# Kernel optimization log

Hardware: AMD Instinct MI355X
Metric: run time of the kernel (lower is better)

## Reference

```python
import jax, jax.numpy as jnp
import numpy as np

NUM_HEADS = 16
HIDDEN = 1024
ATTN_DIM = 64            # per-head q/k dim
HEAD_OUT = 64            # per-head v dim
OUT_DIM = 1024
BATCH, SEQ = 2, 2048


def setup_inputs() -> dict:
    key = jax.random.key(0)
    ks = jax.random.split(key, 9)
    s_in = 1.0 / np.sqrt(HIDDEN)
    s_o = 1.0 / np.sqrt(NUM_HEADS * HEAD_OUT)
    return {
        "x": jax.random.normal(ks[0], (BATCH, SEQ, HIDDEN), dtype=jnp.float32),
        # Linear weights stored [in, out] so y = x @ W + b
        "Wq": jax.random.uniform(ks[1], (HIDDEN, NUM_HEADS * ATTN_DIM), jnp.float32, -s_in, s_in),
        "bq": jax.random.uniform(ks[2], (NUM_HEADS * ATTN_DIM,), jnp.float32, -s_in, s_in),
        "Wk": jax.random.uniform(ks[3], (HIDDEN, NUM_HEADS * ATTN_DIM), jnp.float32, -s_in, s_in),
        "bk": jax.random.uniform(ks[4], (NUM_HEADS * ATTN_DIM,), jnp.float32, -s_in, s_in),
        "Wv": jax.random.uniform(ks[5], (HIDDEN, NUM_HEADS * HEAD_OUT), jnp.float32, -s_in, s_in),
        "bv": jax.random.uniform(ks[6], (HIDDEN, NUM_HEADS * HEAD_OUT)[1:], jnp.float32, -s_in, s_in),
        "Wo": jax.random.uniform(ks[7], (NUM_HEADS * HEAD_OUT, OUT_DIM), jnp.float32, -s_o, s_o),
        "bo": jax.random.uniform(ks[8], (OUT_DIM,), jnp.float32, -s_o, s_o),
    }


def _split_heads(y, h):
    b, s, _ = y.shape
    return y.reshape(b, s, h, -1).transpose(0, 2, 1, 3)  # [b, h, s, d]


def reference(x, Wq, bq, Wk, bk, Wv, bv, Wo, bo):
    h = NUM_HEADS
    q = _split_heads(x @ Wq + bq, h)                    # [b,h,s,dq]
    k = _split_heads(x @ Wk + bk, h)                    # [b,h,s,dq]
    v = _split_heads(x @ Wv + bv, h)                    # [b,h,s,dv]
    scale = 1.0 / jnp.sqrt(jnp.float32(ATTN_DIM))
    # pattern[b,h,i,j] = key_i . query_j  (i=key index, j=query index)
    pattern = jnp.einsum('bhid,bhjd->bhij', k, q) * scale
    # softmax over key axis (dim=-2), matching t.softmax(..., dim=-2)
    prob = jax.nn.softmax(pattern, axis=-2)             # [b,h,key,query]
    # out[b,h,s,d] = sum_i prob[b,h,i,s] * v[b,h,i,d]
    out = jnp.einsum('bhis,bhid->bhsd', prob, v)        # [b,h,s,dv]
    b, _, s, dv = out.shape
    concat = out.transpose(0, 2, 1, 3).reshape(b, s, h * dv)
    return concat @ Wo + bo
```

## Files before the change

### kernel.cpp

```cpp
#include <hip/hip_runtime.h>
#include <cstdint>
#include <cstddef>

using f16   = _Float16;
using f16x4 = __attribute__((ext_vector_type(4))) _Float16;
using f16x8 = __attribute__((ext_vector_type(8))) _Float16;
using f32x4 = __attribute__((ext_vector_type(4))) float;

__device__ __forceinline__ f32x4 mfma16(f16x8 a, f16x8 b, f32x4 c) {
  return __builtin_amdgcn_mfma_f32_16x16x32_f16(a, b, c, 0, 0, 0);
}

__device__ __forceinline__ void gld16(const f16* g, f16* l) {
  __builtin_amdgcn_global_load_lds(
      (__attribute__((address_space(1))) void*)g,
      (__attribute__((address_space(3))) void*)l, 16, 0, 0);
}

constexpr int BATCH = 2, SEQL = 2048, HID = 1024, NH = 16, DH = 64;
constexpr int TOK = BATCH * SEQL;
constexpr int NQKV = 3 * HID;

__global__ __launch_bounds__(256) void k_convert_x(const float* __restrict__ x,
                                                   f16* __restrict__ xh) {
  int i = (blockIdx.x * 256 + threadIdx.x) * 4;
  float4 v = *(const float4*)(x + i);
  f16x4 o = { (f16)v.x, (f16)v.y, (f16)v.z, (f16)v.w };
  *(f16x4*)(xh + i) = o;
}

__global__ __launch_bounds__(256) void k_transpose(const float* __restrict__ Wq,
                                                   const float* __restrict__ Wk,
                                                   const float* __restrict__ Wv,
                                                   const float* __restrict__ Wo,
                                                   f16* __restrict__ WT,
                                                   f16* __restrict__ WoT) {
  __shared__ float tile[32][33];
  int mat = blockIdx.z;
  const float* W = (mat == 0) ? Wq : (mat == 1) ? Wk : (mat == 2) ? Wv : Wo;
  int in0 = blockIdx.x * 32, out0 = blockIdx.y * 32;
  int c = threadIdx.x & 31, r8 = threadIdx.x >> 5;
#pragma unroll
  for (int i = 0; i < 4; i++) {
    int r = r8 + i * 8;
    tile[r][c] = W[(size_t)(in0 + r) * HID + out0 + c];
  }
  __syncthreads();
#pragma unroll
  for (int i = 0; i < 4; i++) {
    int r = r8 + i * 8;
    f16 v = (f16)tile[c][r];
    if (mat == 3) WoT[(size_t)(out0 + r) * HID + in0 + c] = v;
    else          WT[(size_t)(mat * HID + out0 + r) * HID + in0 + c] = v;
  }
}

__global__ __launch_bounds__(256, 2) void k_gemm_qkv(
    const f16* __restrict__ xh, const f16* __restrict__ WT,
    const float* __restrict__ bq, const float* __restrict__ bk,
    const float* __restrict__ bv,
    f16* __restrict__ Qh, f16* __restrict__ Kh, f16* __restrict__ Vth) {
  constexpr int K = HID;
  int m0 = blockIdx.x * 128, n0 = blockIdx.y * 128;
  int tid = threadIdx.x;
  int w = tid >> 6, lane = tid & 63, lr = lane & 15, lq = lane >> 4;
  int wm = w >> 1, wn = w & 1;
  __shared__ f16 Ash[128 * 32];
  __shared__ f16 Bsh[128 * 32];
  f32x4 acc[4][4];
#pragma unroll
  for (int i = 0; i < 4; i++)
#pragma unroll
    for (int j = 0; j < 4; j++) acc[i][j] = (f32x4){0.f, 0.f, 0.f, 0.f};

  int row0 = tid >> 2, seg0 = tid & 3;
  int row1 = (256 + tid) >> 2;
  const f16* Ag0 = xh + (size_t)(m0 + row0) * K + seg0 * 8;
  const f16* Ag1 = xh + (size_t)(m0 + row1) * K + seg0 * 8;
  const f16* Bg0 = WT + (size_t)(n0 + row0) * K + seg0 * 8;
  const f16* Bg1 = WT + (size_t)(n0 + row1) * K + seg0 * 8;

  for (int k0 = 0; k0 < K; k0 += 32) {
    __syncthreads();
    gld16(Ag0 + k0, Ash + tid * 8);
    gld16(Ag1 + k0, Ash + (256 + tid) * 8);
    gld16(Bg0 + k0, Bsh + tid * 8);
    gld16(Bg1 + k0, Bsh + (256 + tid) * 8);
    __syncthreads();
    f16x8 af[4], bfr[4];
#pragma unroll
    for (int mt = 0; mt < 4; mt++)
      af[mt] = *(const f16x8*)(Ash + (wm * 64 + mt * 16 + lr) * 32 + lq * 8);
#pragma unroll
    for (int nt = 0; nt < 4; nt++)
      bfr[nt] = *(const f16x8*)(Bsh + (wn * 64 + nt * 16 + lr) * 32 + lq * 8);
#pragma unroll
    for (int mt = 0; mt < 4; mt++)
#pragma unroll
      for (int nt = 0; nt < 4; nt++)
        acc[mt][nt] = mfma16(af[mt], bfr[nt], acc[mt][nt]);
  }

#pragma unroll
  for (int nt = 0; nt < 4; nt++) {
    int o = n0 + wn * 64 + nt * 16 + lr;
    int sec = o >> 10, o1 = o & 1023, hh = o1 >> 6, dd = o1 & 63;
    float bias = (sec == 0) ? bq[o1] : (sec == 1) ? bk[o1] : bv[o1];
#pragma unroll
    for (int mt = 0; mt < 4; mt++) {
      int t0 = m0 + wm * 64 + mt * 16 + lq * 4;
      int b = t0 >> 11, s0 = t0 & (SEQL - 1);
      size_t bh = (size_t)(b * NH + hh);
      if (sec == 2) {
        f16x4 pv = { (f16)(acc[mt][nt][0] + bias), (f16)(acc[mt][nt][1] + bias),
                     (f16)(acc[mt][nt][2] + bias), (f16)(acc[mt][nt][3] + bias) };
        *(f16x4*)(Vth + (bh * DH + dd) * SEQL + s0) = pv;
      } else {
        f16* dst = (sec == 0) ? Qh : Kh;
#pragma unroll
        for (int r = 0; r < 4; r++)
          dst[(bh * SEQL + s0 + r) * DH + dd] = (f16)(acc[mt][nt][r] + bias);
      }
    }
  }
}

__global__ __launch_bounds__(256, 4) void k_attn(const f16* __restrict__ Qh,
                                                 const f16* __restrict__ Kh,
                                                 const f16* __restrict__ Vth,
                                                 f16* __restrict__ Ao) {
  int qblk = blockIdx.x;
  int bh = blockIdx.y;
  int b = bh >> 4, h = bh & 15;
  int tid = threadIdx.x, w = tid >> 6, lane = tid & 63, lr = lane & 15, lq = lane >> 4;

  __shared__ f16 Ksh[64 * 72];
  __shared__ f16 Vsh[64 * 72];

  int q = qblk * 64 + w * 16 + lr;
  const f16* Qbase = Qh + ((size_t)bh * SEQL + q) * DH;
  f16x8 qf[2];
#pragma unroll
  for (int ks = 0; ks < 2; ks++) {
    qf[ks] = *(const f16x8*)(Qbase + ks * 32 + lq * 8);
    qf[ks] = qf[ks] * (f16)0.125f;
  }

  f32x4 O[4];
#pragma unroll
  for (int dt = 0; dt < 4; dt++) O[dt] = (f32x4){0.f, 0.f, 0.f, 0.f};
  float lsum = 0.f;

  int srow = tid >> 3, sseg = tid & 7;
  int srow1 = (256 + tid) >> 3;
  const f16* Kg0 = Kh + ((size_t)bh * SEQL + srow) * DH + sseg * 8;
  const f16* Kg1 = Kh + ((size_t)bh * SEQL + srow1) * DH + sseg * 8;
  const f16* Vg0 = Vth + ((size_t)bh * DH + srow) * SEQL + sseg * 8;
  const f16* Vg1 = Vth + ((size_t)bh * DH + srow1) * SEQL + sseg * 8;

  for (int kb = 0; kb < SEQL / 64; kb++) {
    __syncthreads();
    *(uint4*)(Ksh + srow * 72 + sseg * 8)  = *(const uint4*)(Kg0 + (size_t)kb * 64 * DH);
    *(uint4*)(Ksh + srow1 * 72 + sseg * 8) = *(const uint4*)(Kg1 + (size_t)kb * 64 * DH);
    *(uint4*)(Vsh + srow * 72 + sseg * 8)  = *(const uint4*)(Vg0 + kb * 64);
    *(uint4*)(Vsh + srow1 * 72 + sseg * 8) = *(const uint4*)(Vg1 + kb * 64);
    __syncthreads();

    f32x4 sacc[4];
#pragma unroll
    for (int kt = 0; kt < 4; kt++) sacc[kt] = (f32x4){0.f, 0.f, 0.f, 0.f};
#pragma unroll
    for (int ks = 0; ks < 2; ks++) {
#pragma unroll
      for (int kt = 0; kt < 4; kt++) {
        f16x8 kf = *(const f16x8*)(Ksh + (kt * 16 + lr) * 72 + ks * 32 + lq * 8);
        sacc[kt] = mfma16(kf, qf[ks], sacc[kt]);
      }
    }

    f16x8 pf[2];
    float part = 0.f;
#pragma unroll
    for (int kt = 0; kt < 4; kt++) {
      float p0 = __expf(sacc[kt][0]);
      float p1 = __expf(sacc[kt][1]);
      float p2 = __expf(sacc[kt][2]);
      float p3 = __expf(sacc[kt][3]);
      part += (p0 + p1) + (p2 + p3);
      int s = kt >> 1, off = (kt & 1) * 4;
      pf[s][off + 0] = (f16)p0; pf[s][off + 1] = (f16)p1;
      pf[s][off + 2] = (f16)p2; pf[s][off + 3] = (f16)p3;
    }
    lsum += part;

#pragma unroll
    for (int s = 0; s < 2; s++) {
#pragma unroll
      for (int dt = 0; dt < 4; dt++) {
        const f16* vb = Vsh + (dt * 16 + lr) * 72 + s * 32 + lq * 4;
        f16x4 v0 = *(const f16x4*)(vb);
        f16x4 v1 = *(const f16x4*)(vb + 16);
        f16x8 vf = { v0[0], v0[1], v0[2], v0[3], v1[0], v1[1], v1[2], v1[3] };
        O[dt] = mfma16(vf, pf[s], O[dt]);
      }
    }
  }

  float l1 = lsum + __shfl_xor(lsum, 16);
  float ltot = l1 + __shfl_xor(l1, 32);
  float inv = 1.0f / ltot;
  f16* dst = Ao + ((size_t)b * SEQL + q) * HID + h * DH;
#pragma unroll
  for (int dt = 0; dt < 4; dt++) {
    f16x4 o = { (f16)(O[dt][0] * inv), (f16)(O[dt][1] * inv),
                (f16)(O[dt][2] * inv), (f16)(O[dt][3] * inv) };
    *(f16x4*)(dst + dt * 16 + lq * 4) = o;
  }
}

__global__ __launch_bounds__(256, 2) void k_gemm_out(const f16* __restrict__ Ah,
                                                     const f16* __restrict__ WoT,
                                                     const float* __restrict__ bo,
                                                     float* __restrict__ out) {
  constexpr int K = HID;
  int m0 = blockIdx.x * 128, n0 = blockIdx.y * 64;
  int tid = threadIdx.x;
  int w = tid >> 6, lane = tid & 63, lr = lane & 15, lq = lane >> 4;
  int wm = w >> 1, wn = w & 1;
  __shared__ f16 Ash[128 * 32];
  __shared__ f16 Bsh[64 * 32];
  f32x4 acc[4][2];
#pragma unroll
  for (int i = 0; i < 4; i++)
#pragma unroll
    for (int j = 0; j < 2; j++) acc[i][j] = (f32x4){0.f, 0.f, 0.f, 0.f};

  int row0 = tid >> 2, seg0 = tid & 3;
  int row1 = (256 + tid) >> 2;
  const f16* Ag0 = Ah + (size_t)(m0 + row0) * K + seg0 * 8;
  const f16* Ag1 = Ah + (size_t)(m0 + row1) * K + seg0 * 8;
  const f16* Bg0 = WoT + (size_t)(n0 + row0) * K + seg0 * 8;

  for (int k0 = 0; k0 < K; k0 += 32) {
    __syncthreads();
    gld16(Ag0 + k0, Ash + tid * 8);
    gld16(Ag1 + k0, Ash + (256 + tid) * 8);
    gld16(Bg0 + k0, Bsh + tid * 8);
    __syncthreads();
    f16x8 af[4], bfr[2];
#pragma unroll
    for (int mt = 0; mt < 4; mt++)
      af[mt] = *(const f16x8*)(Ash + (wm * 64 + mt * 16 + lr) * 32 + lq * 8);
#pragma unroll
    for (int nt = 0; nt < 2; nt++)
      bfr[nt] = *(const f16x8*)(Bsh + (wn * 32 + nt * 16 + lr) * 32 + lq * 8);
#pragma unroll
    for (int mt = 0; mt < 4; mt++)
#pragma unroll
      for (int nt = 0; nt < 2; nt++)
        acc[mt][nt] = mfma16(af[mt], bfr[nt], acc[mt][nt]);
  }

#pragma unroll
  for (int nt = 0; nt < 2; nt++) {
    int o = n0 + wn * 32 + nt * 16 + lr;
    float bias = bo[o];
#pragma unroll
    for (int mt = 0; mt < 4; mt++) {
      int t0 = m0 + wm * 64 + mt * 16 + lq * 4;
#pragma unroll
      for (int r = 0; r < 4; r++)
        out[(size_t)(t0 + r) * HID + o] = acc[mt][nt][r] + bias;
    }
  }
}

extern "C" void kernel_launch(void* const* d_in, const int* in_sizes, int n_in,
                              void* d_out, int out_size, void* d_ws, size_t ws_size,
                              hipStream_t stream) {
  const float* x  = (const float*)d_in[0];
  const float* Wq = (const float*)d_in[1];
  const float* bq = (const float*)d_in[2];
  const float* Wk = (const float*)d_in[3];
  const float* bk = (const float*)d_in[4];
  const float* Wv = (const float*)d_in[5];
  const float* bv = (const float*)d_in[6];
  const float* Wo = (const float*)d_in[7];
  const float* bo = (const float*)d_in[8];

  char* ws = (char*)d_ws;
  f16* xh  = (f16*)(ws + 0);
  f16* WT  = (f16*)(ws + 8388608);
  f16* WoT = (f16*)(ws + 14680064);
  f16* Qh  = (f16*)(ws + 16777216);
  f16* Kh  = (f16*)(ws + 25165824);
  f16* Vth = (f16*)(ws + 33554432);
  f16* Ao  = (f16*)(ws + 41943040);

  k_convert_x<<<TOK * HID / 1024, 256, 0, stream>>>(x, xh);
  k_transpose<<<dim3(32, 32, 4), 256, 0, stream>>>(Wq, Wk, Wv, Wo, WT, WoT);
  k_gemm_qkv<<<dim3(TOK / 128, NQKV / 128), 256, 0, stream>>>(xh, WT, bq, bk, bv,
                                                              Qh, Kh, Vth);
  k_attn<<<dim3(SEQL / 64, BATCH * NH), 256, 0, stream>>>(Qh, Kh, Vth, Ao);
  k_gemm_out<<<dim3(TOK / 128, HID / 64), 256, 0, stream>>>(Ao, WoT, bo,
                                                            (float*)d_out);
}
```

Measured before the change: 207.5 us.

## Double-buffer attention K/V tiles, process two query tiles per wave, permute V layout

The attention kernel now handles 128 queries per block, with each wave computing two 16-query tiles that share the same K and V fragments loaded from LDS. K/V loads are register-prefetched into a double-buffered LDS tile, which removes one barrier per iteration. The V layout written by the QKV GEMM is permuted so the PV operand becomes one contiguous 8-element LDS load instead of two 4-element loads. exp is replaced with exp2 by folding log2(e) into the Q scale. The cost is more registers and lower occupancy, with launch bounds reduced to 2 blocks per SM, and the grid is reordered so that blockIdx.x indexes the head.

```diff
diff --git a/kernel.cpp b/kernel.cpp
--- a/kernel.cpp
+++ b/kernel.cpp
@@ -59,7 +59,7 @@
     const f16* __restrict__ xh, const f16* __restrict__ WT,
     const float* __restrict__ bq, const float* __restrict__ bk,
     const float* __restrict__ bv,
-    f16* __restrict__ Qh, f16* __restrict__ Kh, f16* __restrict__ Vth) {
+    f16* __restrict__ Qh, f16* __restrict__ Kh, f16* __restrict__ Vp) {
   constexpr int K = HID;
   int m0 = blockIdx.x * 128, n0 = blockIdx.y * 128;
   int tid = threadIdx.x;
@@ -114,7 +114,8 @@
       if (sec == 2) {
         f16x4 pv = { (f16)(acc[mt][nt][0] + bias), (f16)(acc[mt][nt][1] + bias),
                      (f16)(acc[mt][nt][2] + bias), (f16)(acc[mt][nt][3] + bias) };
-        *(f16x4*)(Vth + (bh * DH + dd) * SEQL + s0) = pv;
+        int pb = (s0 & ~31) | ((s0 & 12) << 1) | ((s0 >> 2) & 4);
+        *(f16x4*)(Vp + (bh * DH + dd) * SEQL + pb) = pv;
       } else {
         f16* dst = (sec == 0) ? Qh : Kh;
 #pragma unroll
@@ -125,96 +126,120 @@
   }
 }
 
-__global__ __launch_bounds__(256, 4) void k_attn(const f16* __restrict__ Qh,
+__global__ __launch_bounds__(256, 2) void k_attn(const f16* __restrict__ Qh,
                                                  const f16* __restrict__ Kh,
-                                                 const f16* __restrict__ Vth,
+                                                 const f16* __restrict__ Vp,
                                                  f16* __restrict__ Ao) {
-  int qblk = blockIdx.x;
-  int bh = blockIdx.y;
+  int bh = blockIdx.x;
+  int qblk = blockIdx.y;
   int b = bh >> 4, h = bh & 15;
   int tid = threadIdx.x, w = tid >> 6, lane = tid & 63, lr = lane & 15, lq = lane >> 4;
 
-  __shared__ f16 Ksh[64 * 72];
-  __shared__ f16 Vsh[64 * 72];
-
-  int q = qblk * 64 + w * 16 + lr;
-  const f16* Qbase = Qh + ((size_t)bh * SEQL + q) * DH;
-  f16x8 qf[2];
-#pragma unroll
-  for (int ks = 0; ks < 2; ks++) {
-    qf[ks] = *(const f16x8*)(Qbase + ks * 32 + lq * 8);
-    qf[ks] = qf[ks] * (f16)0.125f;
-  }
-
-  f32x4 O[4];
-#pragma unroll
-  for (int dt = 0; dt < 4; dt++) O[dt] = (f32x4){0.f, 0.f, 0.f, 0.f};
-  float lsum = 0.f;
-
-  int srow = tid >> 3, sseg = tid & 7;
-  int srow1 = (256 + tid) >> 3;
+  __shared__ f16 Ksh[2][64 * 72];
+  __shared__ f16 Vsh[2][64 * 72];
+
+  f16x8 qf[2][2];
+#pragma unroll
+  for (int qt = 0; qt < 2; qt++) {
+    const f16* Qbase =
+        Qh + ((size_t)bh * SEQL + qblk * 128 + w * 32 + qt * 16 + lr) * DH;
+#pragma unroll
+    for (int ks = 0; ks < 2; ks++) {
+      qf[qt][ks] = *(const f16x8*)(Qbase + ks * 32 + lq * 8);
+      qf[qt][ks] = qf[qt][ks] * (f16)0.18033688f;
+    }
+  }
+
+  f32x4 O[2][4];
+#pragma unroll
+  for (int qt = 0; qt < 2; qt++)
+#pragma unroll
+    for (int dt = 0; dt < 4; dt++) O[qt][dt] = (f32x4){0.f, 0.f, 0.f, 0.f};
+  float lsum[2] = {0.f, 0.f};
+
+  int srow = tid >> 3, sseg = tid & 7, srow1 = srow + 32;
   const f16* Kg0 = Kh + ((size_t)bh * SEQL + srow) * DH + sseg * 8;
   const f16* Kg1 = Kh + ((size_t)bh * SEQL + srow1) * DH + sseg * 8;
-  const f16* Vg0 = Vth + ((size_t)bh * DH + srow) * SEQL + sseg * 8;
-  const f16* Vg1 = Vth + ((size_t)bh * DH + srow1) * SEQL + sseg * 8;
+  const f16* Vg0 = Vp + ((size_t)bh * DH + srow) * SEQL + sseg * 8;
+  const f16* Vg1 = Vp + ((size_t)bh * DH + srow1) * SEQL + sseg * 8;
+
+  uint4 kr0 = *(const uint4*)(Kg0), kr1 = *(const uint4*)(Kg1);
+  uint4 vr0 = *(const uint4*)(Vg0), vr1 = *(const uint4*)(Vg1);
 
   for (int kb = 0; kb < SEQL / 64; kb++) {
-    __syncthreads();
-    *(uint4*)(Ksh + srow * 72 + sseg * 8)  = *(const uint4*)(Kg0 + (size_t)kb * 64 * DH);
-    *(uint4*)(Ksh + srow1 * 72 + sseg * 8) = *(const uint4*)(Kg1 + (size_t)kb * 64 * DH);
-    *(uint4*)(Vsh + srow * 72 + sseg * 8)  = *(const uint4*)(Vg0 + kb * 64);
-    *(uint4*)(Vsh + srow1 * 72 + sseg * 8) = *(const uint4*)(Vg1 + kb * 64);
-    __syncthreads();
-
-    f32x4 sacc[4];
-#pragma unroll
-    for (int kt = 0; kt < 4; kt++) sacc[kt] = (f32x4){0.f, 0.f, 0.f, 0.f};
+    f16* Kp = Ksh[kb & 1];
+    f16* Vq = Vsh[kb & 1];
+    *(uint4*)(Kp + srow * 72 + sseg * 8) = kr0;
+    *(uint4*)(Kp + srow1 * 72 + sseg * 8) = kr1;
+    *(uint4*)(Vq + srow * 72 + sseg * 8) = vr0;
+    *(uint4*)(Vq + srow1 * 72 + sseg * 8) = vr1;
+    if (kb < SEQL / 64 - 1) {
+      size_t ko = (size_t)(kb + 1) * 64 * DH;
+      int vo = (kb + 1) * 64;
+      kr0 = *(const uint4*)(Kg0 + ko);
+      kr1 = *(const uint4*)(Kg1 + ko);
+      vr0 = *(const uint4*)(Vg0 + vo);
+      vr1 = *(const uint4*)(Vg1 + vo);
+    }
+    __syncthreads();
+
+    f32x4 sacc[2][4];
+#pragma unroll
+    for (int qt = 0; qt < 2; qt++)
+#pragma unroll
+      for (int kt = 0; kt < 4; kt++) sacc[qt][kt] = (f32x4){0.f, 0.f, 0.f, 0.f};
 #pragma unroll
     for (int ks = 0; ks < 2; ks++) {
 #pragma unroll
       for (int kt = 0; kt < 4; kt++) {
-        f16x8 kf = *(const f16x8*)(Ksh + (kt * 16 + lr) * 72 + ks * 32 + lq * 8);
-        sacc[kt] = mfma16(kf, qf[ks], sacc[kt]);
+        f16x8 kf = *(const f16x8*)(Kp + (kt * 16 + lr) * 72 + ks * 32 + lq * 8);
+        sacc[0][kt] = mfma16(kf, qf[0][ks], sacc[0][kt]);
+        sacc[1][kt] = mfma16(kf, qf[1][ks], sacc[1][kt]);
       }
     }
 
-    f16x8 pf[2];
-    float part = 0.f;
-#pragma unroll
-    for (int kt = 0; kt < 4; kt++) {
-      float p0 = __expf(sacc[kt][0]);
-      float p1 = __expf(sacc[kt][1]);
-      float p2 = __expf(sacc[kt][2]);
-      float p3 = __expf(sacc[kt][3]);
-      part += (p0 + p1) + (p2 + p3);
-      int s = kt >> 1, off = (kt & 1) * 4;
-      pf[s][off + 0] = (f16)p0; pf[s][off + 1] = (f16)p1;
-      pf[s][off + 2] = (f16)p2; pf[s][off + 3] = (f16)p3;
-    }
-    lsum += part;
+    f16x8 pf[2][2];
+#pragma unroll
+    for (int qt = 0; qt < 2; qt++) {
+      float part = 0.f;
+#pragma unroll
+      for (int kt = 0; kt < 4; kt++) {
+        float p0 = __builtin_amdgcn_exp2f(sacc[qt][kt][0]);
+        float p1 = __builtin_amdgcn_exp2f(sacc[qt][kt][1]);
+        float p2 = __builtin_amdgcn_exp2f(sacc[qt][kt][2]);
+        float p3 = __builtin_amdgcn_exp2f(sacc[qt][kt][3]);
+        part += (p0 + p1) + (p2 + p3);
+        int s = kt >> 1, off = (kt & 1) * 4;
+        pf[qt][s][off + 0] = (f16)p0; pf[qt][s][off + 1] = (f16)p1;
+        pf[qt][s][off + 2] = (f16)p2; pf[qt][s][off + 3] = (f16)p3;
+      }
+      lsum[qt] += part;
+    }
 
 #pragma unroll
     for (int s = 0; s < 2; s++) {
 #pragma unroll
       for (int dt = 0; dt < 4; dt++) {
-        const f16* vb = Vsh + (dt * 16 + lr) * 72 + s * 32 + lq * 4;
-        f16x4 v0 = *(const f16x4*)(vb);
-        f16x4 v1 = *(const f16x4*)(vb + 16);
-        f16x8 vf = { v0[0], v0[1], v0[2], v0[3], v1[0], v1[1], v1[2], v1[3] };
-        O[dt] = mfma16(vf, pf[s], O[dt]);
+        f16x8 vf = *(const f16x8*)(Vq + (dt * 16 + lr) * 72 + s * 32 + lq * 8);
+        O[0][dt] = mfma16(vf, pf[0][s], O[0][dt]);
+        O[1][dt] = mfma16(vf, pf[1][s], O[1][dt]);
       }
     }
   }
 
-  float l1 = lsum + __shfl_xor(lsum, 16);
-  float ltot = l1 + __shfl_xor(l1, 32);
-  float inv = 1.0f / ltot;
-  f16* dst = Ao + ((size_t)b * SEQL + q) * HID + h * DH;
-#pragma unroll
-  for (int dt = 0; dt < 4; dt++) {
-    f16x4 o = { (f16)(O[dt][0] * inv), (f16)(O[dt][1] * inv),
-                (f16)(O[dt][2] * inv), (f16)(O[dt][3] * inv) };
-    *(f16x4*)(dst + dt * 16 + lq * 4) = o;
+#pragma unroll
+  for (int qt = 0; qt < 2; qt++) {
+    float l1 = lsum[qt] + __shfl_xor(lsum[qt], 16);
+    float ltot = l1 + __shfl_xor(l1, 32);
+    float inv = 1.0f / ltot;
+    int q = qblk * 128 + w * 32 + qt * 16 + lr;
+    f16* dst = Ao + ((size_t)b * SEQL + q) * HID + h * DH;
+#pragma unroll
+    for (int dt = 0; dt < 4; dt++) {
+      f16x4 o = { (f16)(O[qt][dt][0] * inv), (f16)(O[qt][dt][1] * inv),
+                  (f16)(O[qt][dt][2] * inv), (f16)(O[qt][dt][3] * inv) };
+      *(f16x4*)(dst + dt * 16 + lq * 4) = o;
+    }
   }
 }
 
@@ -294,14 +319,14 @@
   f16* WoT = (f16*)(ws + 14680064);
   f16* Qh  = (f16*)(ws + 16777216);
   f16* Kh  = (f16*)(ws + 25165824);
-  f16* Vth = (f16*)(ws + 33554432);
+  f16* Vp  = (f16*)(ws + 33554432);
   f16* Ao  = (f16*)(ws + 41943040);
 
   k_convert_x<<<TOK * HID / 1024, 256, 0, stream>>>(x, xh);
   k_transpose<<<dim3(32, 32, 4), 256, 0, stream>>>(Wq, Wk, Wv, Wo, WT, WoT);
   k_gemm_qkv<<<dim3(TOK / 128, NQKV / 128), 256, 0, stream>>>(xh, WT, bq, bk, bv,
-                                                              Qh, Kh, Vth);
-  k_attn<<<dim3(SEQL / 64, BATCH * NH), 256, 0, stream>>>(Qh, Kh, Vth, Ao);
+                                                              Qh, Kh, Vp);
+  k_attn<<<dim3(BATCH * NH, SEQL / 128), 256, 0, stream>>>(Qh, Kh, Vp, Ao);
   k_gemm_out<<<dim3(TOK / 128, HID / 64), 256, 0, stream>>>(Ao, WoT, bo,
                                                             (float*)d_out);
 }
```

Result: faster. 187.7 us (-9.5%).
